# Optimization experiments

Measured on AMD Instinct MI355X. Metric: run time of the kernel, lower is better.

The kernel has to match this reference:

```python
import jax, jax.numpy as jnp
import numpy as np

BS = 1
H_ = 200
W_ = 200
NQ = H_ * W_          # 40000 BEV queries == num_value
D = 256
NH = 8
DH = D // NH          # 32
NL = 1
NP = 4
NQUEUE = 2
B2 = BS * NQUEUE


def setup_inputs() -> dict:
    key = jax.random.key(0)
    ks = jax.random.split(key, 12)
    s = 0.02
    inp = {
        "query": jax.random.normal(ks[0], (BS, NQ, D), jnp.float32),
        "query_pos": jax.random.normal(ks[1], (BS, NQ, D), jnp.float32) * 0.1,
        "reference_points": jax.random.uniform(ks[2], (BS, NQ, NL, 2), jnp.float32),
        # sampling_offsets linear: in = d_model*num_bev_queue, out = queue*heads*levels*points*2
        "W_so": jax.random.normal(ks[3], (D * NQUEUE, NQUEUE * NH * NL * NP * 2), jnp.float32) * s,
        "b_so": jax.random.normal(ks[4], (NQUEUE * NH * NL * NP * 2,), jnp.float32),
        # attention_weights linear: out = queue*heads*levels*points
        "W_aw": jax.random.normal(ks[5], (D * NQUEUE, NQUEUE * NH * NL * NP), jnp.float32) * s,
        "b_aw": jax.random.normal(ks[6], (NQUEUE * NH * NL * NP,), jnp.float32) * s,
        "W_v": jax.random.normal(ks[7], (D, D), jnp.float32) * s,
        "b_v": jax.random.normal(ks[8], (D,), jnp.float32) * s,
        "W_o": jax.random.normal(ks[9], (D, D), jnp.float32) * s,
        "b_o": jax.random.normal(ks[10], (D,), jnp.float32) * s,
    }
    return inp


def _deform_attn_single_level(v, loc, attn_w):
    """v: (B, Nv, NH, DH); loc: (B, Nq, NH, NP, 2) in [0,1]; attn_w: (B, Nq, NH, NP).
    grid_sample semantics: align_corners=False, zero padding."""
    B = v.shape[0]
    vt = v.transpose(0, 2, 1, 3)                      # (B, NH, Nv, DH)
    # pixel coords (align_corners=False): p = loc * size - 0.5
    x = (loc[..., 0] * W_ - 0.5).transpose(0, 2, 1, 3).reshape(B, NH, -1)  # (B, NH, Nq*NP)
    y = (loc[..., 1] * H_ - 0.5).transpose(0, 2, 1, 3).reshape(B, NH, -1)
    wt = attn_w.transpose(0, 2, 1, 3).reshape(B, NH, -1)
    x0f = jnp.floor(x); y0f = jnp.floor(y)
    x0 = x0f.astype(jnp.int32); y0 = y0f.astype(jnp.int32)
    x1 = x0 + 1; y1 = y0 + 1
    wx1 = x - x0f; wx0 = 1.0 - wx1
    wy1 = y - y0f; wy0 = 1.0 - wy1

    def corner(ix, iy, cw):
        valid = (ix >= 0) & (ix < W_) & (iy >= 0) & (iy < H_)
        idx = jnp.clip(iy, 0, H_ - 1) * W_ + jnp.clip(ix, 0, W_ - 1)
        g = jnp.take_along_axis(vt, idx[..., None], axis=2)   # (B, NH, Nq*NP, DH)
        return g * (cw * valid.astype(cw.dtype))[..., None]

    acc = (corner(x0, y0, wx0 * wy0) + corner(x1, y0, wx1 * wy0)
           + corner(x0, y1, wx0 * wy1) + corner(x1, y1, wx1 * wy1))
    acc = acc * wt[..., None]
    acc = acc.reshape(B, NH, -1, NP, DH).sum(3)               # (B, NH, Nq, DH)
    return acc.transpose(0, 2, 1, 3).reshape(B, -1, NH * DH)  # (B, Nq, D)


def reference(query, query_pos, reference_points, W_so, b_so, W_aw, b_aw, W_v, b_v, W_o, b_o):
    # input_flatten defaults to query (pre-positional); query gets pos added
    q = query + query_pos
    # default queue construction: duplicate current BEV -> (bs*queue, Nv, D)
    value = jnp.stack([query, query], axis=1).reshape(B2, NQ, D)
    history_bev = value[:BS]                                   # (bs, Nv, D)
    qwh = jnp.concatenate([history_bev, q], axis=-1)           # (bs, Nq, 2D)
    # value projection
    v = (value @ W_v + b_v).reshape(B2, NQ, NH, DH)
    # offsets / weights from concatenated features
    so = (qwh @ W_so + b_so).reshape(BS, NQ, NH, NQUEUE, NL, NP, 2)
    aw = (qwh @ W_aw + b_aw).reshape(BS, NQ, NH, NQUEUE, NL * NP)
    aw = jax.nn.softmax(aw, axis=-1).reshape(BS, NQ, NH, NQUEUE, NL, NP)
    aw = aw.transpose(0, 3, 1, 2, 4, 5).reshape(B2, NQ, NH, NL, NP)
    so = so.transpose(0, 3, 1, 2, 4, 5, 6).reshape(B2, NQ, NH, NL, NP, 2)
    # duplicate reference points across the queue
    rp = jnp.stack([reference_points] * NQUEUE, axis=1).reshape(B2, NQ, NL, 2)
    offset_norm = jnp.array([W_, H_], jnp.float32)             # (w, h)
    loc = rp[:, :, None, :, None, :] + so / offset_norm        # (B2, NQ, NH, NL, NP, 2)
    out = _deform_attn_single_level(v, loc[:, :, :, 0], aw[:, :, :, 0])  # (B2, NQ, D)
    # fuse queue outputs by mean (queue is the fast axis of B2)
    out = out.reshape(BS, NQUEUE, NQ, D).mean(axis=1)
    return out @ W_o + b_o
```

## Files before the change

kernel.cpp:

```cpp
#include <hip/hip_runtime.h>
#include <math.h>

#define NQc 40000
#define Wc 200
#define Hc 200

typedef __attribute__((ext_vector_type(8))) short short8;
typedef __attribute__((ext_vector_type(4))) float f32x4;
typedef __attribute__((ext_vector_type(2))) float f32x2;

__device__ __forceinline__ ushort f2b(float f) {
  unsigned u = __float_as_uint(f);
  u = (u + 0x7fffu + ((u >> 16) & 1u)) >> 16;
  return (ushort)u;
}

__device__ __forceinline__ void glds16(const void* g, void* l) {
  __builtin_amdgcn_global_load_lds(
      (const __attribute__((address_space(1))) void*)g,
      (__attribute__((address_space(3))) void*)l, 16, 0, 0);
}

__global__ __launch_bounds__(256) void prep_w(
    const float* __restrict__ Wv, const float* __restrict__ Wo,
    const float* __restrict__ Wso, const float* __restrict__ Waw,
    ushort* __restrict__ WvT, ushort* __restrict__ WoT,
    ushort* __restrict__ WsoT, ushort* __restrict__ WawT) {
  const int idx = blockIdx.x * 256 + threadIdx.x;
  if (idx < 65536) {
    int n = idx >> 8, k = idx & 255;
    WvT[idx] = f2b(Wv[k * 256 + n]);
  } else if (idx < 131072) {
    int i = idx - 65536;
    int n = i >> 8, k = i & 255;
    WoT[i] = f2b(Wo[k * 256 + n]);
  } else if (idx < 196608) {
    int i = idx - 131072;
    int n = i >> 9, k = i & 511;
    WsoT[i] = f2b(Wso[k * 128 + n]);
  } else {
    int i = idx - 196608;
    int n = i >> 9, k = i & 511;
    WawT[i] = f2b(Waw[k * 64 + n]);
  }
}


__global__ __launch_bounds__(256, 3) void gemm_soaw_k(
    const float* __restrict__ q, const float* __restrict__ qp,
    const ushort* __restrict__ WsoT, const ushort* __restrict__ WawT,
    const float* __restrict__ b_so, const float* __restrict__ b_aw,
    float* __restrict__ so_ws, float* __restrict__ aw_ws) {
  __shared__ __align__(16) char smem[33792];
  ushort (*As)[72] = (ushort(*)[72])smem;
  ushort* BsU = (ushort*)(smem + 9216);
  float (*E)[68] = (float(*)[68])smem;
  f32x4 acc[12] = {};
  const int m0 = blockIdx.x * 64;
  const int tid = threadIdx.x;
  const int w = tid >> 6, lane = tid & 63;
  const int rl = lane & 15, q2 = lane >> 4;
  const int sw8 = rl & 7;
  const int lrow = lane >> 3, lch = (lane & 7) ^ (lrow & 7);
  const int arow = tid >> 2, ac16 = (tid & 3) * 16;
  const float* qrow  = q  + (size_t)(m0 + arow) * 256 + ac16;
  const float* qprow = qp + (size_t)(m0 + arow) * 256 + ac16;

  float4 f[4], g4[4];
#pragma unroll
  for (int i = 0; i < 4; ++i) f[i] = *(const float4*)(qrow + i * 4);

  for (int k0 = 0; k0 < 512; k0 += 64) {
    const bool hi = (k0 >= 256);
    __syncthreads();
#pragma unroll
    for (int i = 0; i < 6; ++i) {
      const int g = w * 6 + i;
      const int row = g * 8 + lrow;
      const ushort* gsrc = (row < 128)
          ? WsoT + (size_t)row * 512 + k0 + lch * 8
          : WawT + (size_t)(row - 128) * 512 + k0 + lch * 8;
      glds16(gsrc, BsU + g * 512 + lane * 8);
    }
    {
      ushort tmp[16];
#pragma unroll
      for (int i = 0; i < 4; ++i) {
        float4 a = f[i];
        if (hi) { float4 b = g4[i]; a.x += b.x; a.y += b.y; a.z += b.z; a.w += b.w; }
        tmp[i * 4 + 0] = f2b(a.x); tmp[i * 4 + 1] = f2b(a.y);
        tmp[i * 4 + 2] = f2b(a.z); tmp[i * 4 + 3] = f2b(a.w);
      }
      *(uint4*)&As[arow][ac16]     = *(const uint4*)&tmp[0];
      *(uint4*)&As[arow][ac16 + 8] = *(const uint4*)&tmp[8];
    }
    __syncthreads();
    if (k0 + 64 < 512) {
      const int kn = k0 + 64;
      const int kq = (kn >= 256) ? kn - 256 : kn;
#pragma unroll
      for (int i = 0; i < 4; ++i) f[i] = *(const float4*)(qrow + kq + i * 4);
      if (kn >= 256) {
#pragma unroll
        for (int i = 0; i < 4; ++i) g4[i] = *(const float4*)(qprow + kq + i * 4);
      }
    }
#pragma unroll
    for (int kk = 0; kk < 2; ++kk) {
      const short8 af = *(const short8*)&As[w * 16 + rl][kk * 32 + q2 * 8];
#pragma unroll
      for (int nj = 0; nj < 12; ++nj) {
        const short8 bf = *(const short8*)
            &BsU[(nj * 16 + rl) * 64 + ((kk * 4 + q2) ^ sw8) * 8];
        acc[nj] = __builtin_amdgcn_mfma_f32_16x16x32_bf16(af, bf, acc[nj], 0, 0, 0);
      }
    }
  }
  __syncthreads();

  const int rbase = q2 * 4, cl = rl;
#pragma unroll
  for (int p = 0; p < 3; ++p) {
#pragma unroll
    for (int j = 0; j < 4; ++j) {
      const int nj = p * 4 + j;
      const int nl = j * 16 + cl;
      const f32x4 a = acc[nj];
      if (p < 2) {
        const float bb = b_so[p * 64 + nl];
#pragma unroll
        for (int r = 0; r < 4; ++r)
          E[w * 16 + rbase + r][nl] = a[r] + bb;
      } else {
        const float bb = b_aw[nl];
#pragma unroll
        for (int r = 0; r < 4; ++r) {
          float z = a[r] + bb;
          float zm = fmaxf(z, __shfl_xor(z, 1, 64));
          zm = fmaxf(zm, __shfl_xor(zm, 2, 64));
          float e = expf(z - zm);
          float s = e + __shfl_xor(e, 1, 64);
          s = s + __shfl_xor(s, 2, 64);
          E[w * 16 + rbase + r][nl] = e / s;
        }
      }
    }
    __syncthreads();
#pragma unroll
    for (int it = 0; it < 4; ++it) {
      const int flat = it * 256 + tid;
      const int row = flat >> 4, c4 = (flat & 15) * 4;
      const float4 vle = *(const float4*)&E[row][c4];
      if (p < 2)
        *(float4*)&so_ws[(size_t)(m0 + row) * 128 + p * 64 + c4] = vle;
      else
        *(float4*)&aw_ws[(size_t)(m0 + row) * 64 + c4] = vle;
    }
    __syncthreads();
  }
}

__global__ __launch_bounds__(256, 3) void gemm_v_k(
    const float* __restrict__ q, const ushort* __restrict__ WvT,
    const float* __restrict__ bv, ushort* __restrict__ vt) {
  __shared__ __align__(16) char smem[25600];
  ushort (*As)[72] = (ushort(*)[72])smem;
  ushort* BsU = (ushort*)(smem + 9216);
  ushort (*Eb)[72] = (ushort(*)[72])smem;
  f32x4 acc[8] = {};
  const int m0 = blockIdx.x * 64, n0 = blockIdx.y * 128;
  const int tid = threadIdx.x;
  const int w = tid >> 6, lane = tid & 63;
  const int rl = lane & 15, q2 = lane >> 4;
  const int sw8 = rl & 7;
  const int lrow = lane >> 3, lch = (lane & 7) ^ (lrow & 7);
  const int arow = tid >> 2, ac16 = (tid & 3) * 16;
  const float* qrow = q + (size_t)(m0 + arow) * 256 + ac16;

  float4 f[4];
#pragma unroll
  for (int i = 0; i < 4; ++i) f[i] = *(const float4*)(qrow + i * 4);

  for (int k0 = 0; k0 < 256; k0 += 64) {
    __syncthreads();
#pragma unroll
    for (int i = 0; i < 4; ++i) {
      const int g = w * 4 + i;
      const int row = g * 8 + lrow;
      glds16(WvT + (size_t)(n0 + row) * 256 + k0 + lch * 8,
             BsU + g * 512 + lane * 8);
    }
    {
      ushort tmp[16];
#pragma unroll
      for (int i = 0; i < 4; ++i) {
        const float4 a = f[i];
        tmp[i * 4 + 0] = f2b(a.x); tmp[i * 4 + 1] = f2b(a.y);
        tmp[i * 4 + 2] = f2b(a.z); tmp[i * 4 + 3] = f2b(a.w);
      }
      *(uint4*)&As[arow][ac16]     = *(const uint4*)&tmp[0];
      *(uint4*)&As[arow][ac16 + 8] = *(const uint4*)&tmp[8];
    }
    __syncthreads();
    if (k0 + 64 < 256) {
#pragma unroll
      for (int i = 0; i < 4; ++i) f[i] = *(const float4*)(qrow + k0 + 64 + i * 4);
    }
#pragma unroll
    for (int kk = 0; kk < 2; ++kk) {
      const short8 af = *(const short8*)&As[w * 16 + rl][kk * 32 + q2 * 8];
#pragma unroll
      for (int nj = 0; nj < 8; ++nj) {
        const short8 bf = *(const short8*)
            &BsU[(nj * 16 + rl) * 64 + ((kk * 4 + q2) ^ sw8) * 8];
        acc[nj] = __builtin_amdgcn_mfma_f32_16x16x32_bf16(af, bf, acc[nj], 0, 0, 0);
      }
    }
  }
  __syncthreads();

  const int rbase = q2 * 4, cl = rl;
#pragma unroll
  for (int p = 0; p < 2; ++p) {
#pragma unroll
    for (int j = 0; j < 4; ++j) {
      const int nj = p * 4 + j;
      const int n = n0 + p * 64 + j * 16 + cl;
      const float bb = bv[n];
      const f32x4 a = acc[nj];
#pragma unroll
      for (int r = 0; r < 4; ++r)
        Eb[w * 16 + rbase + r][j * 16 + cl] = f2b(a[r] + bb);
    }
    __syncthreads();
#pragma unroll
    for (int hh = 0; hh < 2; ++hh) {
      const int h = (n0 + p * 64) / 32 + hh;
#pragma unroll
      for (int it = 0; it < 2; ++it) {
        const int flat = it * 256 + tid;
        const int row = flat >> 3, d4 = (flat & 7) * 4;
        *(ushort4*)&vt[((size_t)h * NQc + m0 + row) * 32 + d4] =
            *(const ushort4*)&Eb[row][hh * 32 + d4];
      }
    }
    __syncthreads();
  }
}

__global__ __launch_bounds__(256, 4) void gemm_o_k(
    const ushort* __restrict__ Ap, const ushort* __restrict__ WoT,
    const float* __restrict__ bo, float* __restrict__ out) {
  __shared__ __align__(16) char smem[24576];
  ushort* AsU = (ushort*)smem;
  ushort* BsU = (ushort*)(smem + 8192);
  float (*E)[68] = (float(*)[68])smem;
  f32x4 acc[8] = {};
  const int m0 = blockIdx.x * 64, n0 = blockIdx.y * 128;
  const int tid = threadIdx.x;
  const int w = tid >> 6, lane = tid & 63;
  const int rl = lane & 15, q2 = lane >> 4;
  const int sw8 = rl & 7;
  const int lrow = lane >> 3, lch = (lane & 7) ^ (lrow & 7);

  for (int k0 = 0; k0 < 256; k0 += 64) {
    __syncthreads();
#pragma unroll
    for (int i = 0; i < 2; ++i) {
      const int g = w * 2 + i;
      const int row = g * 8 + lrow;
      glds16(Ap + (size_t)(m0 + row) * 256 + k0 + lch * 8,
             AsU + g * 512 + lane * 8);
    }
#pragma unroll
    for (int i = 0; i < 4; ++i) {
      const int g = w * 4 + i;
      const int row = g * 8 + lrow;
      glds16(WoT + (size_t)(n0 + row) * 256 + k0 + lch * 8,
             BsU + g * 512 + lane * 8);
    }
    __syncthreads();
#pragma unroll
    for (int kk = 0; kk < 2; ++kk) {
      const short8 af = *(const short8*)
          &AsU[(w * 16 + rl) * 64 + ((kk * 4 + q2) ^ sw8) * 8];
#pragma unroll
      for (int nj = 0; nj < 8; ++nj) {
        const short8 bf = *(const short8*)
            &BsU[(nj * 16 + rl) * 64 + ((kk * 4 + q2) ^ sw8) * 8];
        acc[nj] = __builtin_amdgcn_mfma_f32_16x16x32_bf16(af, bf, acc[nj], 0, 0, 0);
      }
    }
  }
  __syncthreads();

  const int rbase = q2 * 4, cl = rl;
#pragma unroll
  for (int p = 0; p < 2; ++p) {
#pragma unroll
    for (int j = 0; j < 4; ++j) {
      const int nj = p * 4 + j;
      const int n = n0 + p * 64 + j * 16 + cl;
      const float bb = bo[n];
      const f32x4 a = acc[nj];
#pragma unroll
      for (int r = 0; r < 4; ++r)
        E[w * 16 + rbase + r][j * 16 + cl] = a[r] + bb;
    }
    __syncthreads();
#pragma unroll
    for (int it = 0; it < 4; ++it) {
      const int flat = it * 256 + tid;
      const int row = flat >> 4, c4 = (flat & 15) * 4;
      *(float4*)&out[(size_t)(m0 + row) * 256 + n0 + p * 64 + c4] =
          *(const float4*)&E[row][c4];
    }
    __syncthreads();
  }
}

__global__ __launch_bounds__(256) void sample_kernel(
    const ushort* __restrict__ vt,
    const float* __restrict__ so_ws,
    const float* __restrict__ aw_ws,
    const float* __restrict__ refp,
    ushort* __restrict__ out_pre)
{
  __shared__ int2   offs[32][9];
  __shared__ float2 wts2[32][9][2];
  const int h  = blockIdx.x & 7;
  const int m0 = (blockIdx.x >> 3) * 32;
  const int tid = threadIdx.x;

  {
    const int j  = tid & 7;
    const int qi = tid >> 3;
    const int m  = m0 + qi;
    const int c  = h * 8 + j;
    const float sx  = so_ws[(size_t)m * 128 + c * 2 + 0];
    const float sy  = so_ws[(size_t)m * 128 + c * 2 + 1];
    const float wgt = 0.5f * aw_ws[(size_t)m * 64 + c];
    const float x = refp[m * 2 + 0] * (float)Wc + sx - 0.5f;
    const float y = refp[m * 2 + 1] * (float)Hc + sy - 0.5f;
    const float x0f = floorf(x), y0f = floorf(y);
    const int x0 = (int)x0f, y0 = (int)y0f;
    const int x1 = x0 + 1, y1 = y0 + 1;
    const float wx1 = x - x0f, wx0 = 1.0f - wx1;
    const float wy1 = y - y0f, wy0 = 1.0f - wy1;
    const float wx0v = (x0 >= 0 && x0 < Wc) ? wx0 : 0.0f;
    const float wx1v = (x1 >= 0 && x1 < Wc) ? wx1 : 0.0f;
    const float wy0v = ((y0 >= 0 && y0 < Hc) ? wy0 : 0.0f) * wgt;
    const float wy1v = ((y1 >= 0 && y1 < Hc) ? wy1 : 0.0f) * wgt;
    const int bx = min(max(x0, 0), Wc - 2);
    const float wl = (bx == x0) ? wx0v : ((bx == x1) ? wx1v : 0.0f);
    const float wr = (bx + 1 == x1) ? wx1v : ((bx + 1 == x0) ? wx0v : 0.0f);
    const int cy0 = min(max(y0, 0), Hc - 1);
    const int cy1 = min(max(y1, 0), Hc - 1);
    offs[qi][j] = make_int2((cy0 * Wc + bx) * 64, (cy1 * Wc + bx) * 64);
    wts2[qi][j][0] = make_float2(wl * wy0v, wl * wy1v);
    wts2[qi][j][1] = make_float2(wr * wy0v, wr * wy1v);
  }
  __syncthreads();

  const int qi = tid >> 3;
  const int ld = tid & 7;
  const int m  = m0 + qi;
  const int hf = ld >> 2;
  const char* __restrict__ vb = (const char*)(vt + (size_t)h * NQc * 32);
  const uint lo16 = (uint)(ld * 16);

  uint4 raw[16];
#pragma unroll
  for (int j = 0; j < 8; ++j) {
    const int2 oo = offs[qi][j];
    raw[2 * j]     = *(const uint4*)(vb + (uint)oo.x + lo16);
    raw[2 * j + 1] = *(const uint4*)(vb + (uint)oo.y + lo16);
  }

  f32x2 acc0 = {0.0f, 0.0f}, acc1 = {0.0f, 0.0f};
  f32x2 acc2 = {0.0f, 0.0f}, acc3 = {0.0f, 0.0f};

#pragma unroll
  for (int j = 0; j < 8; ++j) {
    const float2 wp = wts2[qi][j][hf];
#pragma unroll
    for (int r = 0; r < 2; ++r) {
      const uint4 rawv = raw[2 * j + r];
      const float w = (r == 0) ? wp.x : wp.y;
      const f32x2 wv = {w, w};
      f32x2 v0, v1, v2, v3;
      v0.x = __uint_as_float(rawv.x << 16);
      v0.y = __uint_as_float(rawv.x & 0xFFFF0000u);
      v1.x = __uint_as_float(rawv.y << 16);
      v1.y = __uint_as_float(rawv.y & 0xFFFF0000u);
      v2.x = __uint_as_float(rawv.z << 16);
      v2.y = __uint_as_float(rawv.z & 0xFFFF0000u);
      v3.x = __uint_as_float(rawv.w << 16);
      v3.y = __uint_as_float(rawv.w & 0xFFFF0000u);
#if __has_builtin(__builtin_elementwise_fma)
      acc0 = __builtin_elementwise_fma(wv, v0, acc0);
      acc1 = __builtin_elementwise_fma(wv, v1, acc1);
      acc2 = __builtin_elementwise_fma(wv, v2, acc2);
      acc3 = __builtin_elementwise_fma(wv, v3, acc3);
#else
      acc0.x = fmaf(w, v0.x, acc0.x); acc0.y = fmaf(w, v0.y, acc0.y);
      acc1.x = fmaf(w, v1.x, acc1.x); acc1.y = fmaf(w, v1.y, acc1.y);
      acc2.x = fmaf(w, v2.x, acc2.x); acc2.y = fmaf(w, v2.y, acc2.y);
      acc3.x = fmaf(w, v3.x, acc3.x); acc3.y = fmaf(w, v3.y, acc3.y);
#endif
    }
  }

  float a[8] = {acc0.x, acc0.y, acc1.x, acc1.y,
                acc2.x, acc2.y, acc3.x, acc3.y};
#pragma unroll
  for (int k = 0; k < 8; ++k) a[k] += __shfl_xor(a[k], 4, 64);

  if (hf == 0) {
    ushort rr[8];
#pragma unroll
    for (int k = 0; k < 8; ++k) rr[k] = f2b(a[k]);
    *(uint4*)&out_pre[(size_t)m * 256 + h * 32 + ld * 8] = *(const uint4*)rr;
  }
}

extern "C" void kernel_launch(void* const* d_in, const int* in_sizes, int n_in,
                              void* d_out, int out_size, void* d_ws, size_t ws_size,
                              hipStream_t stream) {
  const float* query     = (const float*)d_in[0];
  const float* query_pos = (const float*)d_in[1];
  const float* refp      = (const float*)d_in[2];
  const float* W_so      = (const float*)d_in[3];
  const float* b_so      = (const float*)d_in[4];
  const float* W_aw      = (const float*)d_in[5];
  const float* b_aw      = (const float*)d_in[6];
  const float* W_v       = (const float*)d_in[7];
  const float* b_v       = (const float*)d_in[8];
  const float* W_o       = (const float*)d_in[9];
  const float* b_o       = (const float*)d_in[10];
  float* out = (float*)d_out;

  char* base = (char*)d_ws;
  ushort* vt      = (ushort*)base;
  float*  so_ws   = (float*)(base + 20480000);
  float*  aw_ws   = (float*)(base + 40960000);
  ushort* out_pre = (ushort*)(base + 51200000);
  ushort* WvT     = (ushort*)(base + 71680000);
  ushort* WoT     = WvT + 65536;
  ushort* WsoT    = WoT + 65536;
  ushort* WawT    = WsoT + 65536;

  prep_w<<<896, 256, 0, stream>>>(W_v, W_o, W_so, W_aw, WvT, WoT, WsoT, WawT);
  gemm_v_k<<<dim3(625, 2), 256, 0, stream>>>(query, WvT, b_v, vt);
  gemm_soaw_k<<<625, 256, 0, stream>>>(query, query_pos, WsoT, WawT,
                                       b_so, b_aw, so_ws, aw_ws);
  sample_kernel<<<10000, 256, 0, stream>>>(vt, so_ws, aw_ws, refp, out_pre);
  gemm_o_k<<<dim3(625, 2), 256, 0, stream>>>(out_pre, WoT, b_o, out);
}
```

Before: 235.7 us.

## Double-buffer LDS tiles in all three GEMM kernels to overlap loads with MFMA

Converts the soaw, v and o projection GEMMs from single-buffered LDS tiles with two barriers per k-step to ping-pong buffers. The next k-slice's global-to-LDS copies and activation loads are issued before the MFMAs on the current slice, leaving one barrier per step. This doubles shared memory use and lowers the occupancy hints in launch bounds. The sampling kernel also folds the lane offset into its base pointer and adds a scheduling barrier so all gathers are issued before the math.

```diff
diff --git a/kernel.cpp b/kernel.cpp
--- a/kernel.cpp
+++ b/kernel.cpp
@@ -46,14 +46,14 @@
 }
 
 
-__global__ __launch_bounds__(256, 3) void gemm_soaw_k(
+__global__ __launch_bounds__(256, 2) void gemm_soaw_k(
     const float* __restrict__ q, const float* __restrict__ qp,
     const ushort* __restrict__ WsoT, const ushort* __restrict__ WawT,
     const float* __restrict__ b_so, const float* __restrict__ b_aw,
     float* __restrict__ so_ws, float* __restrict__ aw_ws) {
-  __shared__ __align__(16) char smem[33792];
-  ushort (*As)[72] = (ushort(*)[72])smem;
-  ushort* BsU = (ushort*)(smem + 9216);
+  __shared__ __align__(16) char smem[67584];
+#define SOAW_AS(b) ((ushort(*)[72])(smem + (b) * 9216))
+#define SOAW_BS(b) ((ushort*)(smem + 18432 + (b) * 24576))
   float (*E)[68] = (float(*)[68])smem;
   f32x4 acc[12] = {};
   const int m0 = blockIdx.x * 64;
@@ -67,22 +67,69 @@
   const float* qprow = qp + (size_t)(m0 + arow) * 256 + ac16;
 
   float4 f[4], g4[4];
+
+#pragma unroll
+  for (int i = 0; i < 6; ++i) {
+    const int g = w * 6 + i;
+    const int row = g * 8 + lrow;
+    const ushort* gsrc = (row < 128)
+        ? WsoT + (size_t)row * 512 + 0 + lch * 8
+        : WawT + (size_t)(row - 128) * 512 + 0 + lch * 8;
+    glds16(gsrc, SOAW_BS(0) + g * 512 + lane * 8);
+  }
 #pragma unroll
   for (int i = 0; i < 4; ++i) f[i] = *(const float4*)(qrow + i * 4);
-
-  for (int k0 = 0; k0 < 512; k0 += 64) {
-    const bool hi = (k0 >= 256);
-    __syncthreads();
-#pragma unroll
-    for (int i = 0; i < 6; ++i) {
-      const int g = w * 6 + i;
-      const int row = g * 8 + lrow;
-      const ushort* gsrc = (row < 128)
-          ? WsoT + (size_t)row * 512 + k0 + lch * 8
-          : WawT + (size_t)(row - 128) * 512 + k0 + lch * 8;
-      glds16(gsrc, BsU + g * 512 + lane * 8);
+  {
+    ushort tmp[16];
+#pragma unroll
+    for (int i = 0; i < 4; ++i) {
+      const float4 a = f[i];
+      tmp[i * 4 + 0] = f2b(a.x); tmp[i * 4 + 1] = f2b(a.y);
+      tmp[i * 4 + 2] = f2b(a.z); tmp[i * 4 + 3] = f2b(a.w);
+    }
+    *(uint4*)&SOAW_AS(0)[arow][ac16]     = *(const uint4*)&tmp[0];
+    *(uint4*)&SOAW_AS(0)[arow][ac16 + 8] = *(const uint4*)&tmp[8];
+  }
+  __syncthreads();
+
+#pragma unroll
+  for (int t = 0; t < 8; ++t) {
+    const int cur = t & 1, nxt = cur ^ 1;
+    if (t < 7) {
+      const int kn = (t + 1) * 64;
+#pragma unroll
+      for (int i = 0; i < 6; ++i) {
+        const int g = w * 6 + i;
+        const int row = g * 8 + lrow;
+        const ushort* gsrc = (row < 128)
+            ? WsoT + (size_t)row * 512 + kn + lch * 8
+            : WawT + (size_t)(row - 128) * 512 + kn + lch * 8;
+        glds16(gsrc, SOAW_BS(nxt) + g * 512 + lane * 8);
+      }
+      const int kq = (kn >= 256) ? kn - 256 : kn;
+#pragma unroll
+      for (int i = 0; i < 4; ++i) f[i] = *(const float4*)(qrow + kq + i * 4);
+      if (kn >= 256) {
+#pragma unroll
+        for (int i = 0; i < 4; ++i) g4[i] = *(const float4*)(qprow + kq + i * 4);
+      }
     }
     {
+      ushort (*Ac)[72] = SOAW_AS(cur);
+      ushort* Bc = SOAW_BS(cur);
+#pragma unroll
+      for (int kk = 0; kk < 2; ++kk) {
+        const short8 af = *(const short8*)&Ac[w * 16 + rl][kk * 32 + q2 * 8];
+#pragma unroll
+        for (int nj = 0; nj < 12; ++nj) {
+          const short8 bf = *(const short8*)
+              &Bc[(nj * 16 + rl) * 64 + ((kk * 4 + q2) ^ sw8) * 8];
+          acc[nj] = __builtin_amdgcn_mfma_f32_16x16x32_bf16(af, bf, acc[nj], 0, 0, 0);
+        }
+      }
+    }
+    if (t < 7) {
+      const bool hi = ((t + 1) * 64 >= 256);
       ushort tmp[16];
 #pragma unroll
       for (int i = 0; i < 4; ++i) {
@@ -91,32 +138,11 @@
         tmp[i * 4 + 0] = f2b(a.x); tmp[i * 4 + 1] = f2b(a.y);
         tmp[i * 4 + 2] = f2b(a.z); tmp[i * 4 + 3] = f2b(a.w);
       }
-      *(uint4*)&As[arow][ac16]     = *(const uint4*)&tmp[0];
-      *(uint4*)&As[arow][ac16 + 8] = *(const uint4*)&tmp[8];
-    }
-    __syncthreads();
-    if (k0 + 64 < 512) {
-      const int kn = k0 + 64;
-      const int kq = (kn >= 256) ? kn - 256 : kn;
-#pragma unroll
-      for (int i = 0; i < 4; ++i) f[i] = *(const float4*)(qrow + kq + i * 4);
-      if (kn >= 256) {
-#pragma unroll
-        for (int i = 0; i < 4; ++i) g4[i] = *(const float4*)(qprow + kq + i * 4);
-      }
-    }
-#pragma unroll
-    for (int kk = 0; kk < 2; ++kk) {
-      const short8 af = *(const short8*)&As[w * 16 + rl][kk * 32 + q2 * 8];
-#pragma unroll
-      for (int nj = 0; nj < 12; ++nj) {
-        const short8 bf = *(const short8*)
-            &BsU[(nj * 16 + rl) * 64 + ((kk * 4 + q2) ^ sw8) * 8];
-        acc[nj] = __builtin_amdgcn_mfma_f32_16x16x32_bf16(af, bf, acc[nj], 0, 0, 0);
-      }
-    }
-  }
-  __syncthreads();
+      *(uint4*)&SOAW_AS(nxt)[arow][ac16]     = *(const uint4*)&tmp[0];
+      *(uint4*)&SOAW_AS(nxt)[arow][ac16 + 8] = *(const uint4*)&tmp[8];
+    }
+    __syncthreads();
+  }
 
   const int rbase = q2 * 4, cl = rl;
 #pragma unroll
@@ -158,14 +184,16 @@
     }
     __syncthreads();
   }
+#undef SOAW_AS
+#undef SOAW_BS
 }
 
 __global__ __launch_bounds__(256, 3) void gemm_v_k(
     const float* __restrict__ q, const ushort* __restrict__ WvT,
     const float* __restrict__ bv, ushort* __restrict__ vt) {
-  __shared__ __align__(16) char smem[25600];
-  ushort (*As)[72] = (ushort(*)[72])smem;
-  ushort* BsU = (ushort*)(smem + 9216);
+  __shared__ __align__(16) char smem[51200];
+#define GV_AS(b) ((ushort(*)[72])(smem + (b) * 9216))
+#define GV_BS(b) ((ushort*)(smem + 18432 + (b) * 16384))
   ushort (*Eb)[72] = (ushort(*)[72])smem;
   f32x4 acc[8] = {};
   const int m0 = blockIdx.x * 64, n0 = blockIdx.y * 128;
@@ -178,19 +206,59 @@
   const float* qrow = q + (size_t)(m0 + arow) * 256 + ac16;
 
   float4 f[4];
+
+#pragma unroll
+  for (int i = 0; i < 4; ++i) {
+    const int g = w * 4 + i;
+    const int row = g * 8 + lrow;
+    glds16(WvT + (size_t)(n0 + row) * 256 + 0 + lch * 8,
+           GV_BS(0) + g * 512 + lane * 8);
+  }
 #pragma unroll
   for (int i = 0; i < 4; ++i) f[i] = *(const float4*)(qrow + i * 4);
-
-  for (int k0 = 0; k0 < 256; k0 += 64) {
-    __syncthreads();
+  {
+    ushort tmp[16];
 #pragma unroll
     for (int i = 0; i < 4; ++i) {
-      const int g = w * 4 + i;
-      const int row = g * 8 + lrow;
-      glds16(WvT + (size_t)(n0 + row) * 256 + k0 + lch * 8,
-             BsU + g * 512 + lane * 8);
+      const float4 a = f[i];
+      tmp[i * 4 + 0] = f2b(a.x); tmp[i * 4 + 1] = f2b(a.y);
+      tmp[i * 4 + 2] = f2b(a.z); tmp[i * 4 + 3] = f2b(a.w);
+    }
+    *(uint4*)&GV_AS(0)[arow][ac16]     = *(const uint4*)&tmp[0];
+    *(uint4*)&GV_AS(0)[arow][ac16 + 8] = *(const uint4*)&tmp[8];
+  }
+  __syncthreads();
+
+#pragma unroll
+  for (int t = 0; t < 4; ++t) {
+    const int cur = t & 1, nxt = cur ^ 1;
+    if (t < 3) {
+#pragma unroll
+      for (int i = 0; i < 4; ++i) {
+        const int g = w * 4 + i;
+        const int row = g * 8 + lrow;
+        glds16(WvT + (size_t)(n0 + row) * 256 + (t + 1) * 64 + lch * 8,
+               GV_BS(nxt) + g * 512 + lane * 8);
+      }
+#pragma unroll
+      for (int i = 0; i < 4; ++i)
+        f[i] = *(const float4*)(qrow + (t + 1) * 64 + i * 4);
     }
     {
+      ushort (*Ac)[72] = GV_AS(cur);
+      ushort* Bc = GV_BS(cur);
+#pragma unroll
+      for (int kk = 0; kk < 2; ++kk) {
+        const short8 af = *(const short8*)&Ac[w * 16 + rl][kk * 32 + q2 * 8];
+#pragma unroll
+        for (int nj = 0; nj < 8; ++nj) {
+          const short8 bf = *(const short8*)
+              &Bc[(nj * 16 + rl) * 64 + ((kk * 4 + q2) ^ sw8) * 8];
+          acc[nj] = __builtin_amdgcn_mfma_f32_16x16x32_bf16(af, bf, acc[nj], 0, 0, 0);
+        }
+      }
+    }
+    if (t < 3) {
       ushort tmp[16];
 #pragma unroll
       for (int i = 0; i < 4; ++i) {
@@ -198,26 +266,11 @@
         tmp[i * 4 + 0] = f2b(a.x); tmp[i * 4 + 1] = f2b(a.y);
         tmp[i * 4 + 2] = f2b(a.z); tmp[i * 4 + 3] = f2b(a.w);
       }
-      *(uint4*)&As[arow][ac16]     = *(const uint4*)&tmp[0];
-      *(uint4*)&As[arow][ac16 + 8] = *(const uint4*)&tmp[8];
-    }
-    __syncthreads();
-    if (k0 + 64 < 256) {
-#pragma unroll
-      for (int i = 0; i < 4; ++i) f[i] = *(const float4*)(qrow + k0 + 64 + i * 4);
-    }
-#pragma unroll
-    for (int kk = 0; kk < 2; ++kk) {
-      const short8 af = *(const short8*)&As[w * 16 + rl][kk * 32 + q2 * 8];
-#pragma unroll
-      for (int nj = 0; nj < 8; ++nj) {
-        const short8 bf = *(const short8*)
-            &BsU[(nj * 16 + rl) * 64 + ((kk * 4 + q2) ^ sw8) * 8];
-        acc[nj] = __builtin_amdgcn_mfma_f32_16x16x32_bf16(af, bf, acc[nj], 0, 0, 0);
-      }
-    }
-  }
-  __syncthreads();
+      *(uint4*)&GV_AS(nxt)[arow][ac16]     = *(const uint4*)&tmp[0];
+      *(uint4*)&GV_AS(nxt)[arow][ac16 + 8] = *(const uint4*)&tmp[8];
+    }
+    __syncthreads();
+  }
 
   const int rbase = q2 * 4, cl = rl;
 #pragma unroll
@@ -246,14 +299,16 @@
     }
     __syncthreads();
   }
-}
-
-__global__ __launch_bounds__(256, 4) void gemm_o_k(
+#undef GV_AS
+#undef GV_BS
+}
+
+__global__ __launch_bounds__(256, 3) void gemm_o_k(
     const ushort* __restrict__ Ap, const ushort* __restrict__ WoT,
     const float* __restrict__ bo, float* __restrict__ out) {
-  __shared__ __align__(16) char smem[24576];
-  ushort* AsU = (ushort*)smem;
-  ushort* BsU = (ushort*)(smem + 8192);
+  __shared__ __align__(16) char smem[49152];
+#define GO_AS(b) ((ushort*)(smem + (b) * 8192))
+#define GO_BS(b) ((ushort*)(smem + 16384 + (b) * 16384))
   float (*E)[68] = (float(*)[68])smem;
   f32x4 acc[8] = {};
   const int m0 = blockIdx.x * 64, n0 = blockIdx.y * 128;
@@ -263,36 +318,59 @@
   const int sw8 = rl & 7;
   const int lrow = lane >> 3, lch = (lane & 7) ^ (lrow & 7);
 
-  for (int k0 = 0; k0 < 256; k0 += 64) {
-    __syncthreads();
-#pragma unroll
-    for (int i = 0; i < 2; ++i) {
-      const int g = w * 2 + i;
-      const int row = g * 8 + lrow;
-      glds16(Ap + (size_t)(m0 + row) * 256 + k0 + lch * 8,
-             AsU + g * 512 + lane * 8);
-    }
-#pragma unroll
-    for (int i = 0; i < 4; ++i) {
-      const int g = w * 4 + i;
-      const int row = g * 8 + lrow;
-      glds16(WoT + (size_t)(n0 + row) * 256 + k0 + lch * 8,
-             BsU + g * 512 + lane * 8);
-    }
-    __syncthreads();
-#pragma unroll
-    for (int kk = 0; kk < 2; ++kk) {
-      const short8 af = *(const short8*)
-          &AsU[(w * 16 + rl) * 64 + ((kk * 4 + q2) ^ sw8) * 8];
-#pragma unroll
-      for (int nj = 0; nj < 8; ++nj) {
-        const short8 bf = *(const short8*)
-            &BsU[(nj * 16 + rl) * 64 + ((kk * 4 + q2) ^ sw8) * 8];
-        acc[nj] = __builtin_amdgcn_mfma_f32_16x16x32_bf16(af, bf, acc[nj], 0, 0, 0);
-      }
-    }
+#pragma unroll
+  for (int i = 0; i < 2; ++i) {
+    const int g = w * 2 + i;
+    const int row = g * 8 + lrow;
+    glds16(Ap + (size_t)(m0 + row) * 256 + 0 + lch * 8,
+           GO_AS(0) + g * 512 + lane * 8);
+  }
+#pragma unroll
+  for (int i = 0; i < 4; ++i) {
+    const int g = w * 4 + i;
+    const int row = g * 8 + lrow;
+    glds16(WoT + (size_t)(n0 + row) * 256 + 0 + lch * 8,
+           GO_BS(0) + g * 512 + lane * 8);
   }
   __syncthreads();
+
+#pragma unroll
+  for (int t = 0; t < 4; ++t) {
+    const int cur = t & 1, nxt = cur ^ 1;
+    if (t < 3) {
+      const int kn = (t + 1) * 64;
+#pragma unroll
+      for (int i = 0; i < 2; ++i) {
+        const int g = w * 2 + i;
+        const int row = g * 8 + lrow;
+        glds16(Ap + (size_t)(m0 + row) * 256 + kn + lch * 8,
+               GO_AS(nxt) + g * 512 + lane * 8);
+      }
+#pragma unroll
+      for (int i = 0; i < 4; ++i) {
+        const int g = w * 4 + i;
+        const int row = g * 8 + lrow;
+        glds16(WoT + (size_t)(n0 + row) * 256 + kn + lch * 8,
+               GO_BS(nxt) + g * 512 + lane * 8);
+      }
+    }
+    {
+      ushort* Ac = GO_AS(cur);
+      ushort* Bc = GO_BS(cur);
+#pragma unroll
+      for (int kk = 0; kk < 2; ++kk) {
+        const short8 af = *(const short8*)
+            &Ac[(w * 16 + rl) * 64 + ((kk * 4 + q2) ^ sw8) * 8];
+#pragma unroll
+        for (int nj = 0; nj < 8; ++nj) {
+          const short8 bf = *(const short8*)
+              &Bc[(nj * 16 + rl) * 64 + ((kk * 4 + q2) ^ sw8) * 8];
+          acc[nj] = __builtin_amdgcn_mfma_f32_16x16x32_bf16(af, bf, acc[nj], 0, 0, 0);
+        }
+      }
+    }
+    __syncthreads();
+  }
 
   const int rbase = q2 * 4, cl = rl;
 #pragma unroll
@@ -317,6 +395,8 @@
     }
     __syncthreads();
   }
+#undef GO_AS
+#undef GO_BS
 }
 
 __global__ __launch_bounds__(256) void sample_kernel(
@@ -366,16 +446,17 @@
   const int ld = tid & 7;
   const int m  = m0 + qi;
   const int hf = ld >> 2;
-  const char* __restrict__ vb = (const char*)(vt + (size_t)h * NQc * 32);
-  const uint lo16 = (uint)(ld * 16);
+  const char* __restrict__ vb =
+      (const char*)(vt + (size_t)h * NQc * 32) + (uint)(ld * 16);
 
   uint4 raw[16];
 #pragma unroll
   for (int j = 0; j < 8; ++j) {
     const int2 oo = offs[qi][j];
-    raw[2 * j]     = *(const uint4*)(vb + (uint)oo.x + lo16);
-    raw[2 * j + 1] = *(const uint4*)(vb + (uint)oo.y + lo16);
-  }
+    raw[2 * j]     = *(const uint4*)(vb + (uint)oo.x);
+    raw[2 * j + 1] = *(const uint4*)(vb + (uint)oo.y);
+  }
+  __builtin_amdgcn_sched_barrier(0);
 
   f32x2 acc0 = {0.0f, 0.0f}, acc1 = {0.0f, 0.0f};
   f32x2 acc2 = {0.0f, 0.0f}, acc3 = {0.0f, 0.0f};
```

Result: slower. 245.3 us (+4.0%).

## Pre-convert queries to bf16 and double-buffer all GEMM tiles with async LDS loads

Applied to the files above, without the earlier changes.

A new prep pass converts query and query+query_pos to bf16 once, so the GEMMs load both operands straight into LDS with global_load_lds instead of converting fp32 in registers every K step. All three GEMMs now double-buffer their LDS tiles, with explicit vmcnt waits and raw barriers so the next tile's loads overlap the current MFMAs. Workspace buffers are aliased (qhi/vt, qlo/out_pre), so gemm_soaw is launched before gemm_v to consume qhi before vt overwrites it. The costs are an extra full pass over query, larger LDS per block that lowers occupancy, and the need for the buffer aliasing order to stay correct.

```diff
diff --git a/kernel.cpp b/kernel.cpp
--- a/kernel.cpp
+++ b/kernel.cpp
@@ -8,6 +8,8 @@
 typedef __attribute__((ext_vector_type(8))) short short8;
 typedef __attribute__((ext_vector_type(4))) float f32x4;
 typedef __attribute__((ext_vector_type(2))) float f32x2;
+
+#define VMWAIT(N) asm volatile("s_waitcnt vmcnt(" #N ")" ::: "memory")
 
 __device__ __forceinline__ ushort f2b(float f) {
   unsigned u = __float_as_uint(f);
@@ -21,39 +23,65 @@
       (__attribute__((address_space(3))) void*)l, 16, 0, 0);
 }
 
-__global__ __launch_bounds__(256) void prep_w(
+__global__ __launch_bounds__(256) void prep_all(
+    const float* __restrict__ q, const float* __restrict__ qp,
     const float* __restrict__ Wv, const float* __restrict__ Wo,
     const float* __restrict__ Wso, const float* __restrict__ Waw,
+    ushort* __restrict__ qlo, ushort* __restrict__ qhi,
     ushort* __restrict__ WvT, ushort* __restrict__ WoT,
     ushort* __restrict__ WsoT, ushort* __restrict__ WawT) {
-  const int idx = blockIdx.x * 256 + threadIdx.x;
-  if (idx < 65536) {
-    int n = idx >> 8, k = idx & 255;
-    WvT[idx] = f2b(Wv[k * 256 + n]);
-  } else if (idx < 131072) {
-    int i = idx - 65536;
-    int n = i >> 8, k = i & 255;
-    WoT[i] = f2b(Wo[k * 256 + n]);
-  } else if (idx < 196608) {
-    int i = idx - 131072;
-    int n = i >> 9, k = i & 511;
-    WsoT[i] = f2b(Wso[k * 128 + n]);
+  const int bid = blockIdx.x;
+  if (bid < 10000) {
+    const int flat = bid * 256 + threadIdx.x;
+    const int m = flat >> 6;
+    const int c8 = (flat & 63) * 8;
+    ushort o[8];
+    if (c8 < 256) {
+      const float4 a = *(const float4*)(q + (size_t)m * 256 + c8);
+      const float4 b = *(const float4*)(q + (size_t)m * 256 + c8 + 4);
+      o[0] = f2b(a.x); o[1] = f2b(a.y); o[2] = f2b(a.z); o[3] = f2b(a.w);
+      o[4] = f2b(b.x); o[5] = f2b(b.y); o[6] = f2b(b.z); o[7] = f2b(b.w);
+      *(uint4*)&qlo[(size_t)m * 256 + c8] = *(const uint4*)o;
+    } else {
+      const int c = c8 - 256;
+      const float4 a  = *(const float4*)(q  + (size_t)m * 256 + c);
+      const float4 b  = *(const float4*)(q  + (size_t)m * 256 + c + 4);
+      const float4 ap = *(const float4*)(qp + (size_t)m * 256 + c);
+      const float4 bp = *(const float4*)(qp + (size_t)m * 256 + c + 4);
+      o[0] = f2b(a.x + ap.x); o[1] = f2b(a.y + ap.y);
+      o[2] = f2b(a.z + ap.z); o[3] = f2b(a.w + ap.w);
+      o[4] = f2b(b.x + bp.x); o[5] = f2b(b.y + bp.y);
+      o[6] = f2b(b.z + bp.z); o[7] = f2b(b.w + bp.w);
+      *(uint4*)&qhi[(size_t)m * 256 + c] = *(const uint4*)o;
+    }
   } else {
-    int i = idx - 196608;
-    int n = i >> 9, k = i & 511;
-    WawT[i] = f2b(Waw[k * 64 + n]);
-  }
-}
-
-
-__global__ __launch_bounds__(256, 3) void gemm_soaw_k(
-    const float* __restrict__ q, const float* __restrict__ qp,
+    const int idx = (bid - 10000) * 256 + threadIdx.x;
+    if (idx < 65536) {
+      int n = idx >> 8, k = idx & 255;
+      WvT[idx] = f2b(Wv[k * 256 + n]);
+    } else if (idx < 131072) {
+      int i = idx - 65536;
+      int n = i >> 8, k = i & 255;
+      WoT[i] = f2b(Wo[k * 256 + n]);
+    } else if (idx < 196608) {
+      int i = idx - 131072;
+      int n = i >> 9, k = i & 511;
+      WsoT[i] = f2b(Wso[k * 128 + n]);
+    } else {
+      int i = idx - 196608;
+      int n = i >> 9, k = i & 511;
+      WawT[i] = f2b(Waw[k * 64 + n]);
+    }
+  }
+}
+
+
+__global__ __launch_bounds__(256, 2) void gemm_soaw_k(
+    const ushort* __restrict__ qlo, const ushort* __restrict__ qhi,
     const ushort* __restrict__ WsoT, const ushort* __restrict__ WawT,
     const float* __restrict__ b_so, const float* __restrict__ b_aw,
     float* __restrict__ so_ws, float* __restrict__ aw_ws) {
-  __shared__ __align__(16) char smem[33792];
-  ushort (*As)[72] = (ushort(*)[72])smem;
-  ushort* BsU = (ushort*)(smem + 9216);
+  __shared__ __align__(16) char smem[65536];
   float (*E)[68] = (float(*)[68])smem;
   f32x4 acc[12] = {};
   const int m0 = blockIdx.x * 64;
@@ -62,17 +90,20 @@
   const int rl = lane & 15, q2 = lane >> 4;
   const int sw8 = rl & 7;
   const int lrow = lane >> 3, lch = (lane & 7) ^ (lrow & 7);
-  const int arow = tid >> 2, ac16 = (tid & 3) * 16;
-  const float* qrow  = q  + (size_t)(m0 + arow) * 256 + ac16;
-  const float* qprow = qp + (size_t)(m0 + arow) * 256 + ac16;
-
-  float4 f[4], g4[4];
-#pragma unroll
-  for (int i = 0; i < 4; ++i) f[i] = *(const float4*)(qrow + i * 4);
-
-  for (int k0 = 0; k0 < 512; k0 += 64) {
-    const bool hi = (k0 >= 256);
-    __syncthreads();
+
+  auto STAGE = [&](int buf, int t) {
+    ushort* As = (ushort*)(smem + buf * 32768);
+    ushort* Bs = As + 4096;
+    const int k0 = t * 64;
+    const ushort* aq = (k0 < 256) ? qlo : qhi;
+    const int ka = k0 & 255;
+#pragma unroll
+    for (int i = 0; i < 2; ++i) {
+      const int g = w * 2 + i;
+      const int row = g * 8 + lrow;
+      glds16(aq + (size_t)(m0 + row) * 256 + ka + lch * 8,
+             As + g * 512 + lane * 8);
+    }
 #pragma unroll
     for (int i = 0; i < 6; ++i) {
       const int g = w * 6 + i;
@@ -80,43 +111,38 @@
       const ushort* gsrc = (row < 128)
           ? WsoT + (size_t)row * 512 + k0 + lch * 8
           : WawT + (size_t)(row - 128) * 512 + k0 + lch * 8;
-      glds16(gsrc, BsU + g * 512 + lane * 8);
-    }
+      glds16(gsrc, Bs + g * 512 + lane * 8);
+    }
+  };
+
+  STAGE(0, 0);
+#pragma unroll
+  for (int t = 0; t < 8; ++t) {
+    const int cur = t & 1;
+    if (t < 7) {
+      STAGE(cur ^ 1, t + 1);
+      VMWAIT(8);
+    } else {
+      VMWAIT(0);
+    }
+    __builtin_amdgcn_s_barrier();
     {
-      ushort tmp[16];
-#pragma unroll
-      for (int i = 0; i < 4; ++i) {
-        float4 a = f[i];
-        if (hi) { float4 b = g4[i]; a.x += b.x; a.y += b.y; a.z += b.z; a.w += b.w; }
-        tmp[i * 4 + 0] = f2b(a.x); tmp[i * 4 + 1] = f2b(a.y);
-        tmp[i * 4 + 2] = f2b(a.z); tmp[i * 4 + 3] = f2b(a.w);
+      const ushort* Asb = (const ushort*)(smem + cur * 32768);
+      const ushort* Bsb = Asb + 4096;
+#pragma unroll
+      for (int kk = 0; kk < 2; ++kk) {
+        const short8 af = *(const short8*)
+            &Asb[(w * 16 + rl) * 64 + ((kk * 4 + q2) ^ sw8) * 8];
+#pragma unroll
+        for (int nj = 0; nj < 12; ++nj) {
+          const short8 bf = *(const short8*)
+              &Bsb[(nj * 16 + rl) * 64 + ((kk * 4 + q2) ^ sw8) * 8];
+          acc[nj] = __builtin_amdgcn_mfma_f32_16x16x32_bf16(af, bf, acc[nj], 0, 0, 0);
+        }
       }
-      *(uint4*)&As[arow][ac16]     = *(const uint4*)&tmp[0];
-      *(uint4*)&As[arow][ac16 + 8] = *(const uint4*)&tmp[8];
-    }
-    __syncthreads();
-    if (k0 + 64 < 512) {
-      const int kn = k0 + 64;
-      const int kq = (kn >= 256) ? kn - 256 : kn;
-#pragma unroll
-      for (int i = 0; i < 4; ++i) f[i] = *(const float4*)(qrow + kq + i * 4);
-      if (kn >= 256) {
-#pragma unroll
-        for (int i = 0; i < 4; ++i) g4[i] = *(const float4*)(qprow + kq + i * 4);
-      }
-    }
-#pragma unroll
-    for (int kk = 0; kk < 2; ++kk) {
-      const short8 af = *(const short8*)&As[w * 16 + rl][kk * 32 + q2 * 8];
-#pragma unroll
-      for (int nj = 0; nj < 12; ++nj) {
-        const short8 bf = *(const short8*)
-            &BsU[(nj * 16 + rl) * 64 + ((kk * 4 + q2) ^ sw8) * 8];
-        acc[nj] = __builtin_amdgcn_mfma_f32_16x16x32_bf16(af, bf, acc[nj], 0, 0, 0);
-      }
-    }
-  }
-  __syncthreads();
+    }
+    __builtin_amdgcn_s_barrier();
+  }
 
   const int rbase = q2 * 4, cl = rl;
 #pragma unroll
@@ -161,11 +187,9 @@
 }
 
 __global__ __launch_bounds__(256, 3) void gemm_v_k(
-    const float* __restrict__ q, const ushort* __restrict__ WvT,
+    const ushort* __restrict__ qlo, const ushort* __restrict__ WvT,
     const float* __restrict__ bv, ushort* __restrict__ vt) {
-  __shared__ __align__(16) char smem[25600];
-  ushort (*As)[72] = (ushort(*)[72])smem;
-  ushort* BsU = (ushort*)(smem + 9216);
+  __shared__ __align__(16) char smem[49152];
   ushort (*Eb)[72] = (ushort(*)[72])smem;
   f32x4 acc[8] = {};
   const int m0 = blockIdx.x * 64, n0 = blockIdx.y * 128;
@@ -174,50 +198,55 @@
   const int rl = lane & 15, q2 = lane >> 4;
   const int sw8 = rl & 7;
   const int lrow = lane >> 3, lch = (lane & 7) ^ (lrow & 7);
-  const int arow = tid >> 2, ac16 = (tid & 3) * 16;
-  const float* qrow = q + (size_t)(m0 + arow) * 256 + ac16;
-
-  float4 f[4];
-#pragma unroll
-  for (int i = 0; i < 4; ++i) f[i] = *(const float4*)(qrow + i * 4);
-
-  for (int k0 = 0; k0 < 256; k0 += 64) {
-    __syncthreads();
+
+  auto STAGE = [&](int buf, int t) {
+    ushort* As = (ushort*)(smem + buf * 24576);
+    ushort* Bs = As + 4096;
+    const int k0 = t * 64;
+#pragma unroll
+    for (int i = 0; i < 2; ++i) {
+      const int g = w * 2 + i;
+      const int row = g * 8 + lrow;
+      glds16(qlo + (size_t)(m0 + row) * 256 + k0 + lch * 8,
+             As + g * 512 + lane * 8);
+    }
 #pragma unroll
     for (int i = 0; i < 4; ++i) {
       const int g = w * 4 + i;
       const int row = g * 8 + lrow;
       glds16(WvT + (size_t)(n0 + row) * 256 + k0 + lch * 8,
-             BsU + g * 512 + lane * 8);
-    }
+             Bs + g * 512 + lane * 8);
+    }
+  };
+
+  STAGE(0, 0);
+#pragma unroll
+  for (int t = 0; t < 4; ++t) {
+    const int cur = t & 1;
+    if (t < 3) {
+      STAGE(cur ^ 1, t + 1);
+      VMWAIT(6);
+    } else {
+      VMWAIT(0);
+    }
+    __builtin_amdgcn_s_barrier();
     {
-      ushort tmp[16];
-#pragma unroll
-      for (int i = 0; i < 4; ++i) {
-        const float4 a = f[i];
-        tmp[i * 4 + 0] = f2b(a.x); tmp[i * 4 + 1] = f2b(a.y);
-        tmp[i * 4 + 2] = f2b(a.z); tmp[i * 4 + 3] = f2b(a.w);
+      const ushort* Asb = (const ushort*)(smem + cur * 24576);
+      const ushort* Bsb = Asb + 4096;
+#pragma unroll
+      for (int kk = 0; kk < 2; ++kk) {
+        const short8 af = *(const short8*)
+            &Asb[(w * 16 + rl) * 64 + ((kk * 4 + q2) ^ sw8) * 8];
+#pragma unroll
+        for (int nj = 0; nj < 8; ++nj) {
+          const short8 bf = *(const short8*)
+              &Bsb[(nj * 16 + rl) * 64 + ((kk * 4 + q2) ^ sw8) * 8];
+          acc[nj] = __builtin_amdgcn_mfma_f32_16x16x32_bf16(af, bf, acc[nj], 0, 0, 0);
+        }
       }
-      *(uint4*)&As[arow][ac16]     = *(const uint4*)&tmp[0];
-      *(uint4*)&As[arow][ac16 + 8] = *(const uint4*)&tmp[8];
-    }
-    __syncthreads();
-    if (k0 + 64 < 256) {
-#pragma unroll
-      for (int i = 0; i < 4; ++i) f[i] = *(const float4*)(qrow + k0 + 64 + i * 4);
-    }
-#pragma unroll
-    for (int kk = 0; kk < 2; ++kk) {
-      const short8 af = *(const short8*)&As[w * 16 + rl][kk * 32 + q2 * 8];
-#pragma unroll
-      for (int nj = 0; nj < 8; ++nj) {
-        const short8 bf = *(const short8*)
-            &BsU[(nj * 16 + rl) * 64 + ((kk * 4 + q2) ^ sw8) * 8];
-        acc[nj] = __builtin_amdgcn_mfma_f32_16x16x32_bf16(af, bf, acc[nj], 0, 0, 0);
-      }
-    }
-  }
-  __syncthreads();
+    }
+    __builtin_amdgcn_s_barrier();
+  }
 
   const int rbase = q2 * 4, cl = rl;
 #pragma unroll
@@ -248,12 +277,10 @@
   }
 }
 
-__global__ __launch_bounds__(256, 4) void gemm_o_k(
+__global__ __launch_bounds__(256, 3) void gemm_o_k(
     const ushort* __restrict__ Ap, const ushort* __restrict__ WoT,
     const float* __restrict__ bo, float* __restrict__ out) {
-  __shared__ __align__(16) char smem[24576];
-  ushort* AsU = (ushort*)smem;
-  ushort* BsU = (ushort*)(smem + 8192);
+  __shared__ __align__(16) char smem[49152];
   float (*E)[68] = (float(*)[68])smem;
   f32x4 acc[8] = {};
   const int m0 = blockIdx.x * 64, n0 = blockIdx.y * 128;
@@ -263,36 +290,54 @@
   const int sw8 = rl & 7;
   const int lrow = lane >> 3, lch = (lane & 7) ^ (lrow & 7);
 
-  for (int k0 = 0; k0 < 256; k0 += 64) {
-    __syncthreads();
+  auto STAGE = [&](int buf, int t) {
+    ushort* As = (ushort*)(smem + buf * 24576);
+    ushort* Bs = As + 4096;
+    const int k0 = t * 64;
 #pragma unroll
     for (int i = 0; i < 2; ++i) {
       const int g = w * 2 + i;
       const int row = g * 8 + lrow;
       glds16(Ap + (size_t)(m0 + row) * 256 + k0 + lch * 8,
-             AsU + g * 512 + lane * 8);
+             As + g * 512 + lane * 8);
     }
 #pragma unroll
     for (int i = 0; i < 4; ++i) {
       const int g = w * 4 + i;
       const int row = g * 8 + lrow;
       glds16(WoT + (size_t)(n0 + row) * 256 + k0 + lch * 8,
-             BsU + g * 512 + lane * 8);
-    }
-    __syncthreads();
-#pragma unroll
-    for (int kk = 0; kk < 2; ++kk) {
-      const short8 af = *(const short8*)
-          &AsU[(w * 16 + rl) * 64 + ((kk * 4 + q2) ^ sw8) * 8];
-#pragma unroll
-      for (int nj = 0; nj < 8; ++nj) {
-        const short8 bf = *(const short8*)
-            &BsU[(nj * 16 + rl) * 64 + ((kk * 4 + q2) ^ sw8) * 8];
-        acc[nj] = __builtin_amdgcn_mfma_f32_16x16x32_bf16(af, bf, acc[nj], 0, 0, 0);
+             Bs + g * 512 + lane * 8);
+    }
+  };
+
+  STAGE(0, 0);
+#pragma unroll
+  for (int t = 0; t < 4; ++t) {
+    const int cur = t & 1;
+    if (t < 3) {
+      STAGE(cur ^ 1, t + 1);
+      VMWAIT(6);
+    } else {
+      VMWAIT(0);
+    }
+    __builtin_amdgcn_s_barrier();
+    {
+      const ushort* Asb = (const ushort*)(smem + cur * 24576);
+      const ushort* Bsb = Asb + 4096;
+#pragma unroll
+      for (int kk = 0; kk < 2; ++kk) {
+        const short8 af = *(const short8*)
+            &Asb[(w * 16 + rl) * 64 + ((kk * 4 + q2) ^ sw8) * 8];
+#pragma unroll
+        for (int nj = 0; nj < 8; ++nj) {
+          const short8 bf = *(const short8*)
+              &Bsb[(nj * 16 + rl) * 64 + ((kk * 4 + q2) ^ sw8) * 8];
+          acc[nj] = __builtin_amdgcn_mfma_f32_16x16x32_bf16(af, bf, acc[nj], 0, 0, 0);
+        }
       }
     }
-  }
-  __syncthreads();
+    __builtin_amdgcn_s_barrier();
+  }
 
   const int rbase = q2 * 4, cl = rl;
 #pragma unroll
@@ -366,16 +411,17 @@
   const int ld = tid & 7;
   const int m  = m0 + qi;
   const int hf = ld >> 2;
-  const char* __restrict__ vb = (const char*)(vt + (size_t)h * NQc * 32);
-  const uint lo16 = (uint)(ld * 16);
+  const char* __restrict__ vb =
+      (const char*)(vt + (size_t)h * NQc * 32) + (uint)(ld * 16);
 
   uint4 raw[16];
 #pragma unroll
   for (int j = 0; j < 8; ++j) {
     const int2 oo = offs[qi][j];
-    raw[2 * j]     = *(const uint4*)(vb + (uint)oo.x + lo16);
-    raw[2 * j + 1] = *(const uint4*)(vb + (uint)oo.y + lo16);
-  }
+    raw[2 * j]     = *(const uint4*)(vb + (uint)oo.x);
+    raw[2 * j + 1] = *(const uint4*)(vb + (uint)oo.y);
+  }
+  __builtin_amdgcn_sched_barrier(0);
 
   f32x2 acc0 = {0.0f, 0.0f}, acc1 = {0.0f, 0.0f};
   f32x2 acc2 = {0.0f, 0.0f}, acc3 = {0.0f, 0.0f};
@@ -441,19 +487,22 @@
   float* out = (float*)d_out;
 
   char* base = (char*)d_ws;
-  ushort* vt      = (ushort*)base;
-  float*  so_ws   = (float*)(base + 20480000);
-  float*  aw_ws   = (float*)(base + 40960000);
-  ushort* out_pre = (ushort*)(base + 51200000);
+  ushort* qlo     = (ushort*)base;
+  ushort* qhi     = (ushort*)(base + 20480000);
+  ushort* vt      = (ushort*)(base + 20480000);
+  ushort* out_pre = (ushort*)base;
+  float*  so_ws   = (float*)(base + 40960000);
+  float*  aw_ws   = (float*)(base + 61440000);
   ushort* WvT     = (ushort*)(base + 71680000);
   ushort* WoT     = WvT + 65536;
   ushort* WsoT    = WoT + 65536;
   ushort* WawT    = WsoT + 65536;
 
-  prep_w<<<896, 256, 0, stream>>>(W_v, W_o, W_so, W_aw, WvT, WoT, WsoT, WawT);
-  gemm_v_k<<<dim3(625, 2), 256, 0, stream>>>(query, WvT, b_v, vt);
-  gemm_soaw_k<<<625, 256, 0, stream>>>(query, query_pos, WsoT, WawT,
+  prep_all<<<10896, 256, 0, stream>>>(query, query_pos, W_v, W_o, W_so, W_aw,
+                                      qlo, qhi, WvT, WoT, WsoT, WawT);
+  gemm_soaw_k<<<625, 256, 0, stream>>>(qlo, qhi, WsoT, WawT,
                                        b_so, b_aw, so_ws, aw_ws);
+  gemm_v_k<<<dim3(625, 2), 256, 0, stream>>>(qlo, WvT, b_v, vt);
   sample_kernel<<<10000, 256, 0, stream>>>(vt, so_ws, aw_ws, refp, out_pre);
   gemm_o_k<<<dim3(625, 2), 256, 0, stream>>>(out_pre, WoT, b_o, out);
 }
```

Result: faster. 226.6 us (-3.9%).
